# Performance work log

Hardware: AMD Instinct MI355X
Metric: run time of the kernel (lower is better)

Reference implementation:

```python
import jax, jax.numpy as jnp
import numpy as np

N_NODES = 100000
N_EDGES = 1600000
D_IN, D_HID, D_LAT = 128, 128, 64


def setup_inputs() -> dict:
    key = jax.random.key(0)
    ks = jax.random.split(key, 8)
    x = jax.random.normal(ks[0], (N_NODES, D_IN), dtype=jnp.float32)
    edge_index = jax.random.randint(ks[1], (2, N_EDGES), 0, N_NODES, dtype=jnp.int64)
    s1 = 1.0 / np.sqrt(D_IN)
    s2 = 1.0 / np.sqrt(D_HID)
    return {
        "x": x,
        "edge_index": edge_index,
        "W1_l": jax.random.normal(ks[2], (D_IN, D_HID), dtype=jnp.float32) * s1,
        "W1_r": jax.random.normal(ks[3], (D_IN, D_HID), dtype=jnp.float32) * s1,
        "b1": jnp.zeros((D_HID,), dtype=jnp.float32),
        "W2_l": jax.random.normal(ks[4], (D_HID, D_LAT), dtype=jnp.float32) * s2,
        "W2_r": jax.random.normal(ks[5], (D_HID, D_LAT), dtype=jnp.float32) * s2,
        "b2": jnp.zeros((D_LAT,), dtype=jnp.float32),
    }


def _sage_conv_mean(x, src, dst, W_l, W_r, b):
    """PyG SAGEConv with mean aggregation: lin_l(mean_j x_j) + lin_r(x_i)."""
    n = x.shape[0]
    # scatter-mean of source features into destination nodes
    agg = jax.ops.segment_sum(x[src], dst, num_segments=n)           # [N, d]
    deg = jax.ops.segment_sum(jnp.ones_like(dst, dtype=x.dtype), dst, num_segments=n)
    mean = agg / jnp.maximum(deg, 1.0)[:, None]
    return mean @ W_l + b + x @ W_r


def reference(x, edge_index, W1_l, W1_r, b1, W2_l, W2_r, b2):
    src, dst = edge_index[0], edge_index[1]
    h = jax.nn.relu(_sage_conv_mean(x, src, dst, W1_l, W1_r, b1))
    # Dropout(p=0.2) is identity in eval mode
    z = jax.nn.relu(_sage_conv_mean(h, src, dst, W2_l, W2_r, b2))
    return z
```

## Files before the change

### kernel.cpp

```cpp
#include <hip/hip_runtime.h>

#define N_NODES 100000
#define N_EDGES 1600000
#define D_IN 128
#define D_HID 128
#define D_LAT 64

#define BSHIFT 8
#define NB 392
#define CAP 4608
#define EPB 4096
#define PART_BLOCKS ((N_EDGES + EPB - 1) / EPB)
#define CVT_BLOCKS (((long)N_NODES * 128 / 16 + 255) / 256)

typedef unsigned short ushort_t;
typedef unsigned int uint_t;
typedef unsigned char uchar_t;
using bf16x8 = __attribute__((ext_vector_type(8))) short;
using f32x4  = __attribute__((ext_vector_type(4))) float;
using f32x2  = __attribute__((ext_vector_type(2))) float;

__device__ inline ushort_t f2bf(float f) {
    uint_t u = __float_as_uint(f);
    return (ushort_t)((u + 0x7fffu + ((u >> 16) & 1u)) >> 16);
}
__device__ inline uint_t pack2bf(float a, float b) {
    return (uint_t)f2bf(a) | ((uint_t)f2bf(b) << 16);
}
__device__ inline float bf2f(ushort_t u) {
    return __uint_as_float(((uint_t)u) << 16);
}

#if __has_builtin(__builtin_amdgcn_cvt_pk_f32_fp8) && __has_builtin(__builtin_amdgcn_cvt_pk_fp8_f32)
#define HW_FP8 1
template<bool HI>
__device__ inline f32x2 fp8pk2f(uint_t v) {
    return __builtin_amdgcn_cvt_pk_f32_fp8(v, HI);
}
__device__ inline uint_t f2fp8pk4(float a, float b, float c, float d) {
    uint_t w = __builtin_amdgcn_cvt_pk_fp8_f32(a, b, 0, false);
    w = __builtin_amdgcn_cvt_pk_fp8_f32(c, d, w, true);
    return w;
}
__device__ inline uchar_t f2fp8_byte(float f) {
    return (uchar_t)(__builtin_amdgcn_cvt_pk_fp8_f32(f, f, 0, false) & 0xff);
}
#else
__device__ inline float fp8b2f(uint_t b) {
    uint_t em = b & 0x7f;
    if (em == 0) return 0.f;
    uint_t bits = ((em << 20) + (120u << 23)) | ((b & 0x80u) << 24);
    return __uint_as_float(bits);
}
template<bool HI>
__device__ inline f32x2 fp8pk2f(uint_t v) {
    uint_t w = HI ? (v >> 16) : v;
    f32x2 r; r.x = fp8b2f(w & 0xff); r.y = fp8b2f((w >> 8) & 0xff);
    return r;
}
__device__ inline uint_t f2fp8_1(float f) {
    uint_t u = __float_as_uint(f);
    uint_t s = (u >> 31) << 7;
    uint_t au = u & 0x7fffffff;
    if (au >= 0x43e00000u) return s | 0x7e;
    if (au < 0x3c000000u) return s;
    uint_t r = au + 0x0007ffffu + ((au >> 20) & 1u);
    return s | (((r >> 20) - (120u << 3)) & 0x7f);
}
__device__ inline uint_t f2fp8pk4(float a, float b, float c, float d) {
    return f2fp8_1(a) | (f2fp8_1(b) << 8) | (f2fp8_1(c) << 16) | (f2fp8_1(d) << 24);
}
__device__ inline uchar_t f2fp8_byte(float f) { return (uchar_t)f2fp8_1(f); }
#endif

__device__ inline void accf8x4(float* a, uint_t w, int base) {
    f32x2 p0 = fp8pk2f<false>(w);
    f32x2 p1 = fp8pk2f<true>(w);
    a[base + 0] += p0.x; a[base + 1] += p0.y;
    a[base + 2] += p1.x; a[base + 3] += p1.y;
}
__device__ inline void accf8x16(float* a, uint4 u) {
    accf8x4(a, u.x, 0); accf8x4(a, u.y, 4); accf8x4(a, u.z, 8); accf8x4(a, u.w, 12);
}

template<int RSHIFT, int NV, int DEPTH>
__device__ inline void gather_acc_fp8n(const uchar_t* __restrict__ base,
                                       const int* __restrict__ idxp,
                                       int n, float* acc) {
    int k = 0;
    int idx[DEPTH];
    if (n >= DEPTH) {
        #pragma unroll
        for (int j = 0; j < DEPTH; ++j) idx[j] = idxp[j];
    }
    while (k + DEPTH <= n) {
        uint4 u[DEPTH][NV];
        #pragma unroll
        for (int j = 0; j < DEPTH; ++j) {
            #pragma unroll
            for (int v = 0; v < NV; ++v)
                u[j][v] = *(const uint4*)(base + ((long)idx[j] << RSHIFT) + v * 16);
        }
        int kn = k + DEPTH;
        if (kn + DEPTH <= n) {
            #pragma unroll
            for (int j = 0; j < DEPTH; ++j) idx[j] = idxp[kn + j];
        }
        #pragma unroll
        for (int j = 0; j < DEPTH; ++j) {
            #pragma unroll
            for (int v = 0; v < NV; ++v)
                accf8x16(acc + v * 16, u[j][v]);
        }
        k = kn;
    }
    if (k < n) {
        int m = n - k;
        int idr[DEPTH];
        #pragma unroll
        for (int j = 0; j < DEPTH; ++j) {
            int kk = k + j; if (kk > n - 1) kk = n - 1;
            idr[j] = idxp[kk];
        }
        uint4 u[DEPTH][NV];
        #pragma unroll
        for (int j = 0; j < DEPTH; ++j) {
            #pragma unroll
            for (int v = 0; v < NV; ++v)
                u[j][v] = *(const uint4*)(base + ((long)idr[j] << RSHIFT) + v * 16);
        }
        #pragma unroll
        for (int j = 0; j < DEPTH; ++j) {
            if (j < m) {
                #pragma unroll
                for (int v = 0; v < NV; ++v)
                    accf8x16(acc + v * 16, u[j][v]);
            }
        }
    }
}

__device__ inline void pack_w256(const float* Wl, const float* Wr, ushort_t* pack,
                                 int N, int tid) {
    int lane = tid & 63;
    int t = tid >> 6;
    int kt = t & 7;
    int nt = t >> 3;
    int n = nt * 16 + (lane & 15);
    int kbase = kt * 32 + (lane >> 4) * 8;
    ushort_t v[8];
    #pragma unroll
    for (int j = 0; j < 8; ++j) {
        int k = kbase + j;
        float w = (k < 128) ? Wl[k * N + n] : Wr[(k - 128) * N + n];
        v[j] = f2bf(w);
    }
    *(uint4*)(pack + (long)tid * 8) = *(uint4*)v;
}
__device__ inline void pack_w128(const float* W, ushort_t* pack, int N, int tid) {
    int lane = tid & 63;
    int t = tid >> 6;
    int kt = t & 3;
    int nt = t >> 2;
    int n = nt * 16 + (lane & 15);
    int kbase = kt * 32 + (lane >> 4) * 8;
    ushort_t v[8];
    #pragma unroll
    for (int j = 0; j < 8; ++j) v[j] = f2bf(W[(kbase + j) * N + n]);
    *(uint4*)(pack + (long)tid * 8) = *(uint4*)v;
}

__global__ __launch_bounds__(256) void prep_kernel(
        const float* __restrict__ W1_l, const float* __restrict__ W1_r,
        ushort_t* __restrict__ pack1,
        const float* __restrict__ W2_l, ushort_t* __restrict__ pack2l,
        const float* __restrict__ W2_r, ushort_t* __restrict__ pack2r,
        int* __restrict__ gCur,
        const float* __restrict__ x, ushort_t* __restrict__ xb,
        uchar_t* __restrict__ x8) {
    int b = blockIdx.x;
    if (b < 16) {
        pack_w256(W1_l, W1_r, pack1, 128, b * 256 + threadIdx.x);
    } else if (b < 20) {
        pack_w128(W2_l, pack2l, 64, (b - 16) * 256 + threadIdx.x);
    } else if (b < 24) {
        pack_w128(W2_r, pack2r, 64, (b - 20) * 256 + threadIdx.x);
    } else if (b < 26) {
        int t = (b - 24) * 256 + threadIdx.x;
        if (t < NB) gCur[t] = t * CAP;
    } else {
        long i = ((long)(b - 26) * 256 + threadIdx.x) * 16;
        if (i >= (long)N_NODES * 128) return;
        float4 a = *(const float4*)(x + i);
        float4 bb = *(const float4*)(x + i + 4);
        float4 c = *(const float4*)(x + i + 8);
        float4 d = *(const float4*)(x + i + 12);
        uint4 ob0, ob1;
        ob0.x = pack2bf(a.x, a.y);  ob0.y = pack2bf(a.z, a.w);
        ob0.z = pack2bf(bb.x, bb.y); ob0.w = pack2bf(bb.z, bb.w);
        ob1.x = pack2bf(c.x, c.y);  ob1.y = pack2bf(c.z, c.w);
        ob1.z = pack2bf(d.x, d.y);  ob1.w = pack2bf(d.z, d.w);
        *(uint4*)(xb + i) = ob0;
        *(uint4*)(xb + i + 8) = ob1;
        uint4 o8;
        o8.x = f2fp8pk4(a.x, a.y, a.z, a.w);
        o8.y = f2fp8pk4(bb.x, bb.y, bb.z, bb.w);
        o8.z = f2fp8pk4(c.x, c.y, c.z, c.w);
        o8.w = f2fp8pk4(d.x, d.y, d.z, d.w);
        *(uint4*)(x8 + i) = o8;
    }
}

__global__ __launch_bounds__(256) void bucket_scatter_kernel(const int* __restrict__ src,
                                                             const int* __restrict__ dst,
                                                             int* __restrict__ gCur,
                                                             int* __restrict__ bedges) {
    __shared__ int h[NB];
    __shared__ int start[NB];
    for (int j = threadIdx.x; j < NB; j += 256) h[j] = 0;
    __syncthreads();
    long base = (long)blockIdx.x * EPB + threadIdx.x * 16;
    int dc[16], sc[16];
    int cnt = 0;
    if (base + 16 <= N_EDGES) {
        #pragma unroll
        for (int j = 0; j < 4; ++j) {
            int4 d4 = *(const int4*)(dst + base + j * 4);
            int4 s4 = *(const int4*)(src + base + j * 4);
            dc[j * 4 + 0] = d4.x; dc[j * 4 + 1] = d4.y; dc[j * 4 + 2] = d4.z; dc[j * 4 + 3] = d4.w;
            sc[j * 4 + 0] = s4.x; sc[j * 4 + 1] = s4.y; sc[j * 4 + 2] = s4.z; sc[j * 4 + 3] = s4.w;
        }
        cnt = 16;
    } else if (base < N_EDGES) {
        cnt = (int)(N_EDGES - base);
        for (int j = 0; j < cnt; ++j) { dc[j] = dst[base + j]; sc[j] = src[base + j]; }
    }
    for (int j = 0; j < cnt; ++j) atomicAdd(&h[dc[j] >> BSHIFT], 1);
    __syncthreads();
    for (int j = threadIdx.x; j < NB; j += 256)
        start[j] = h[j] ? atomicAdd(&gCur[j], h[j]) : 0;
    __syncthreads();
    for (int j = 0; j < cnt; ++j) {
        int b = dc[j] >> BSHIFT;
        int p = atomicAdd(&start[b], 1);
        if (p < (b + 1) * CAP)
            bedges[p] = ((dc[j] & 255) << 24) | sc[j];
    }
}

__global__ __launch_bounds__(256) void bucket_sort_kernel(const int* __restrict__ gCur,
                                                          const int* __restrict__ bedges,
                                                          int* __restrict__ csr,
                                                          int2* __restrict__ off2) {
    __shared__ int sdata[256];
    __shared__ int cur[256];
    int b = blockIdx.x, t = threadIdx.x;
    int r0 = b * CAP;
    int n = gCur[b] - r0;
    if (n > CAP) n = CAP;
    cur[t] = 0;
    __syncthreads();
    for (int k = t * 4; k < n; k += 1024) {
        int4 v4 = *(const int4*)(bedges + r0 + k);
        int m = n - k;
        atomicAdd(&cur[(unsigned)v4.x >> 24], 1);
        if (m > 1) atomicAdd(&cur[(unsigned)v4.y >> 24], 1);
        if (m > 2) atomicAdd(&cur[(unsigned)v4.z >> 24], 1);
        if (m > 3) atomicAdd(&cur[(unsigned)v4.w >> 24], 1);
    }
    __syncthreads();
    int c = cur[t];
    sdata[t] = c;
    __syncthreads();
    for (int d = 1; d < 256; d <<= 1) {
        int u = (t >= d) ? sdata[t - d] : 0;
        __syncthreads();
        sdata[t] += u;
        __syncthreads();
    }
    int ex = (t == 0) ? 0 : sdata[t - 1];
    off2[(b << BSHIFT) + t] = make_int2(r0 + ex, c);
    cur[t] = ex;
    __syncthreads();
    for (int k = t * 4; k < n; k += 1024) {
        int4 v4 = *(const int4*)(bedges + r0 + k);
        int m = n - k;
        {
            int p = atomicAdd(&cur[(unsigned)v4.x >> 24], 1);
            csr[r0 + p] = v4.x & 0xFFFFFF;
        }
        if (m > 1) {
            int p = atomicAdd(&cur[(unsigned)v4.y >> 24], 1);
            csr[r0 + p] = v4.y & 0xFFFFFF;
        }
        if (m > 2) {
            int p = atomicAdd(&cur[(unsigned)v4.z >> 24], 1);
            csr[r0 + p] = v4.z & 0xFFFFFF;
        }
        if (m > 3) {
            int p = atomicAdd(&cur[(unsigned)v4.w >> 24], 1);
            csr[r0 + p] = v4.w & 0xFFFFFF;
        }
    }
}

#define HSTRIDE 132
__global__ __launch_bounds__(256) void mfma_mlp_fused_kernel(
        const int2* __restrict__ off2, const int* __restrict__ csr_src,
        const uchar_t* __restrict__ x8,
        const ushort_t* __restrict__ Ax,
        const ushort_t* __restrict__ pack1, const float* __restrict__ bias,
        const ushort_t* __restrict__ pack2l,
        ushort_t* __restrict__ hb, uchar_t* __restrict__ g8) {
    __shared__ ushort_t mtile[32 * HSTRIDE];
    __shared__ ushort_t htile[32 * HSTRIDE];
    long m0b = (long)blockIdx.x * 32;
    {
        int lane8 = threadIdx.x & 7;
        int local = threadIdx.x >> 3;
        long i = m0b + local;
        int2 bd = off2[i];
        const uchar_t* gbase = x8 + lane8 * 16;
        float acc[16];
        #pragma unroll
        for (int j = 0; j < 16; ++j) acc[j] = 0.f;
        gather_acc_fp8n<7, 1, 8>(gbase, csr_src + bd.x, bd.y, acc);
        float inv = (bd.y > 0) ? 1.f / (float)bd.y : 0.f;
        uint4 o0, o1;
        o0.x = pack2bf(acc[0] * inv,  acc[1] * inv);
        o0.y = pack2bf(acc[2] * inv,  acc[3] * inv);
        o0.z = pack2bf(acc[4] * inv,  acc[5] * inv);
        o0.w = pack2bf(acc[6] * inv,  acc[7] * inv);
        o1.x = pack2bf(acc[8] * inv,  acc[9] * inv);
        o1.y = pack2bf(acc[10] * inv, acc[11] * inv);
        o1.z = pack2bf(acc[12] * inv, acc[13] * inv);
        o1.w = pack2bf(acc[14] * inv, acc[15] * inv);
        ushort_t* mp = mtile + local * HSTRIDE + lane8 * 16;
        *(uint4*)mp = o0;
        *(uint4*)(mp + 8) = o1;
    }
    __syncthreads();
    int lane = threadIdx.x & 63;
    int wave = threadIdx.x >> 6;
    int wr = wave & 1;
    int wc = wave >> 1;
    int r = lane & 15;
    int quad = lane >> 4;
    int rowl = wr * 16 + r;
    long arow = m0b + rowl;

    bf16x8 areg[8];
    #pragma unroll
    for (int kt = 0; kt < 8; ++kt) {
        int k = (kt & 3) * 32 + quad * 8;
        areg[kt] = (kt < 4)
            ? *(const bf16x8*)(&mtile[rowl * HSTRIDE + k])
            : *(const bf16x8*)(Ax + arow * 128 + k);
    }

    f32x4 acc[4];
    #pragma unroll
    for (int nt = 0; nt < 4; ++nt) acc[nt] = (f32x4){0.f, 0.f, 0.f, 0.f};
    #pragma unroll
    for (int nt = 0; nt < 4; ++nt) {
        int gnt = wc * 4 + nt;
        #pragma unroll
        for (int kt = 0; kt < 8; ++kt) {
            bf16x8 bfrag = *(const bf16x8*)(pack1 + ((long)(gnt * 8 + kt) * 64 + lane) * 8);
            acc[nt] = __builtin_amdgcn_mfma_f32_16x16x32_bf16(areg[kt], bfrag, acc[nt], 0, 0, 0);
        }
    }

    #pragma unroll
    for (int nt = 0; nt < 4; ++nt) {
        int col = wc * 64 + nt * 16 + r;
        float bj = bias[col];
        #pragma unroll
        for (int q = 0; q < 4; ++q) {
            long orow = m0b + wr * 16 + quad * 4 + q;
            float v = fmaxf(acc[nt][q] + bj, 0.f);
            ushort_t hv = f2bf(v);
            hb[orow * 128 + col] = hv;
            htile[(wr * 16 + quad * 4 + q) * HSTRIDE + col] = hv;
        }
    }
    __syncthreads();
    bf16x8 areg2[4];
    #pragma unroll
    for (int kt = 0; kt < 4; ++kt)
        areg2[kt] = *(const bf16x8*)(&htile[rowl * HSTRIDE + kt * 32 + quad * 8]);
    f32x4 gacc[2];
    #pragma unroll
    for (int nt = 0; nt < 2; ++nt) gacc[nt] = (f32x4){0.f, 0.f, 0.f, 0.f};
    #pragma unroll
    for (int nt = 0; nt < 2; ++nt) {
        int gnt = wc * 2 + nt;
        #pragma unroll
        for (int kt = 0; kt < 4; ++kt) {
            bf16x8 bfrag = *(const bf16x8*)(pack2l + ((long)(gnt * 4 + kt) * 64 + lane) * 8);
            gacc[nt] = __builtin_amdgcn_mfma_f32_16x16x32_bf16(areg2[kt], bfrag, gacc[nt], 0, 0, 0);
        }
    }
    #pragma unroll
    for (int nt = 0; nt < 2; ++nt) {
        int col = wc * 32 + nt * 16 + r;
        #pragma unroll
        for (int q = 0; q < 4; ++q) {
            long orow = m0b + wr * 16 + quad * 4 + q;
            g8[orow * 64 + col] = f2fp8_byte(gacc[nt][q]);
        }
    }
}

#define MSTRIDE 68
__global__ __launch_bounds__(256) void mfma_final_kernel(
        const int2* __restrict__ off2, const int* __restrict__ csr_src,
        const uchar_t* __restrict__ g8,
        const ushort_t* __restrict__ hb, const ushort_t* __restrict__ pack2r,
        const float* __restrict__ b2, float* __restrict__ out) {
    __shared__ ushort_t mtile[64 * MSTRIDE];
    long m0 = (long)blockIdx.x * 64;
    {
        int lane  = threadIdx.x & 3;
        int local = threadIdx.x >> 2;
        long i = m0 + local;
        if (i > N_NODES - 1) i = N_NODES - 1;
        int2 bd = off2[i];
        int beg = bd.x, n = bd.y;
        const uchar_t* base = g8 + lane * 16;
        float acc[16];
        #pragma unroll
        for (int j = 0; j < 16; ++j) acc[j] = 0.f;
        gather_acc_fp8n<6, 1, 8>(base, csr_src + beg, n, acc);
        float inv = (n > 0) ? 1.f / (float)n : 0.f;
        uint4 o0, o1;
        o0.x = pack2bf(acc[0] * inv,  acc[1] * inv);
        o0.y = pack2bf(acc[2] * inv,  acc[3] * inv);
        o0.z = pack2bf(acc[4] * inv,  acc[5] * inv);
        o0.w = pack2bf(acc[6] * inv,  acc[7] * inv);
        o1.x = pack2bf(acc[8] * inv,  acc[9] * inv);
        o1.y = pack2bf(acc[10] * inv, acc[11] * inv);
        o1.z = pack2bf(acc[12] * inv, acc[13] * inv);
        o1.w = pack2bf(acc[14] * inv, acc[15] * inv);
        ushort_t* mp = mtile + local * MSTRIDE + lane * 16;
        *(uint4*)mp = o0;
        *(uint4*)(mp + 8) = o1;
    }
    __syncthreads();
    int lane = threadIdx.x & 63;
    int wave = threadIdx.x >> 6;
    long mw = m0 + wave * 16;
    int r = lane & 15;
    int quad = lane >> 4;
    long arow = mw + r;
    if (arow > N_NODES - 1) arow = N_NODES - 1;

    bf16x8 areg[4];
    #pragma unroll
    for (int kt = 0; kt < 4; ++kt)
        areg[kt] = *(const bf16x8*)(hb + arow * 128 + kt * 32 + quad * 8);

    f32x4 acc[4];
    #pragma unroll
    for (int nt = 0; nt < 4; ++nt) {
        int col = nt * 16 + r;
        #pragma unroll
        for (int q = 0; q < 4; ++q) {
            int rowl = wave * 16 + quad * 4 + q;
            acc[nt][q] = bf2f(mtile[rowl * MSTRIDE + col]);
        }
    }
    #pragma unroll
    for (int nt = 0; nt < 4; ++nt) {
        #pragma unroll
        for (int kt = 0; kt < 4; ++kt) {
            bf16x8 bfrag = *(const bf16x8*)(pack2r + ((long)(nt * 4 + kt) * 64 + lane) * 8);
            acc[nt] = __builtin_amdgcn_mfma_f32_16x16x32_bf16(areg[kt], bfrag, acc[nt], 0, 0, 0);
        }
    }
    #pragma unroll
    for (int nt = 0; nt < 4; ++nt) {
        int col = nt * 16 + r;
        float bj = b2[col];
        #pragma unroll
        for (int q = 0; q < 4; ++q) {
            long orow = mw + quad * 4 + q;
            if (orow < N_NODES)
                out[orow * 64 + col] = fmaxf(acc[nt][q] + bj, 0.f);
        }
    }
}

extern "C" void kernel_launch(void* const* d_in, const int* in_sizes, int n_in,
                              void* d_out, int out_size, void* d_ws, size_t ws_size,
                              hipStream_t stream) {
    const float* x    = (const float*)d_in[0];
    const int*   ei   = (const int*)d_in[1];
    const float* W1_l = (const float*)d_in[2];
    const float* W1_r = (const float*)d_in[3];
    const float* b1   = (const float*)d_in[4];
    const float* W2_l = (const float*)d_in[5];
    const float* W2_r = (const float*)d_in[6];
    const float* b2   = (const float*)d_in[7];
    float* out = (float*)d_out;

    const int* src = ei;
    const int* dst = ei + N_EDGES;

    int*  gCur   = (int*)d_ws;
    int2* off2   = (int2*)(gCur + 512);
    int*  bedges = (int*)(off2 + 100608);
    int*  csr    = bedges + NB * CAP;
    ushort_t* xb = (ushort_t*)(csr + NB * CAP);
    ushort_t* hb = xb + (long)N_NODES * 128;
    uchar_t*  x8 = (uchar_t*)(hb + (long)N_NODES * 128);
    ushort_t* pack1  = (ushort_t*)(x8 + (long)N_NODES * 128);
    ushort_t* pack2l = pack1 + 256 * 128;
    ushort_t* pack2r = pack2l + 128 * 64;
    uchar_t*  g8     = (uchar_t*)(pack2r + 128 * 64);

    prep_kernel<<<26 + CVT_BLOCKS, 256, 0, stream>>>(
        W1_l, W1_r, pack1, W2_l, pack2l, W2_r, pack2r, gCur, x, xb, x8);

    bucket_scatter_kernel<<<PART_BLOCKS, 256, 0, stream>>>(src, dst, gCur, bedges);
    bucket_sort_kernel<<<NB, 256, 0, stream>>>(gCur, bedges, csr, off2);

    mfma_mlp_fused_kernel<<<N_NODES / 32, 256, 0, stream>>>(
        off2, csr, x8, xb, pack1, b1, pack2l, hb, g8);

    mfma_final_kernel<<<(N_NODES + 63) / 64, 256, 0, stream>>>(
        off2, csr, g8, hb, pack2r, b2, out);
}
```

Baseline: 232.5 us.

## Fuse layer-2 root projection into layer-1 kernel and split final gather across lanes

The layer-2 root term h@W2_r is now computed in the fused MLP kernel while h is still in shared memory and stored as a 64-wide bf16 tensor. The 128-wide bf16 h buffer is no longer written or re-read. The final kernel becomes a pure gather-mean plus add, bias and relu, with no MFMA. It splits each node's neighbor list across two lane groups with a strided index walk and combines them by shuffle, so more lanes are busy per node. The cost is extra MFMA work and registers in the fused kernel, and a strided index access pattern in the gather.

Measured after the change: 229.1 us. No clear change (-1.5%).

```diff
diff --git a/kernel.cpp b/kernel.cpp
--- a/kernel.cpp
+++ b/kernel.cpp
@@ -83,7 +83,7 @@
     accf8x4(a, u.x, 0); accf8x4(a, u.y, 4); accf8x4(a, u.z, 8); accf8x4(a, u.w, 12);
 }
 
-template<int RSHIFT, int NV, int DEPTH>
+template<int RSHIFT, int NV, int DEPTH, int STRIDE = 1>
 __device__ inline void gather_acc_fp8n(const uchar_t* __restrict__ base,
                                        const int* __restrict__ idxp,
                                        int n, float* acc) {
@@ -91,7 +91,7 @@
     int idx[DEPTH];
     if (n >= DEPTH) {
         #pragma unroll
-        for (int j = 0; j < DEPTH; ++j) idx[j] = idxp[j];
+        for (int j = 0; j < DEPTH; ++j) idx[j] = idxp[j * STRIDE];
     }
     while (k + DEPTH <= n) {
         uint4 u[DEPTH][NV];
@@ -104,7 +104,7 @@
         int kn = k + DEPTH;
         if (kn + DEPTH <= n) {
             #pragma unroll
-            for (int j = 0; j < DEPTH; ++j) idx[j] = idxp[kn + j];
+            for (int j = 0; j < DEPTH; ++j) idx[j] = idxp[(kn + j) * STRIDE];
         }
         #pragma unroll
         for (int j = 0; j < DEPTH; ++j) {
@@ -120,7 +120,7 @@
         #pragma unroll
         for (int j = 0; j < DEPTH; ++j) {
             int kk = k + j; if (kk > n - 1) kk = n - 1;
-            idr[j] = idxp[kk];
+            idr[j] = idxp[kk * STRIDE];
         }
         uint4 u[DEPTH][NV];
         #pragma unroll
@@ -310,8 +310,8 @@
         const uchar_t* __restrict__ x8,
         const ushort_t* __restrict__ Ax,
         const ushort_t* __restrict__ pack1, const float* __restrict__ bias,
-        const ushort_t* __restrict__ pack2l,
-        ushort_t* __restrict__ hb, uchar_t* __restrict__ g8) {
+        const ushort_t* __restrict__ pack2l, const ushort_t* __restrict__ pack2r,
+        ushort_t* __restrict__ f2, uchar_t* __restrict__ g8) {
     __shared__ ushort_t mtile[32 * HSTRIDE];
     __shared__ ushort_t htile[32 * HSTRIDE];
     long m0b = (long)blockIdx.x * 32;
@@ -377,11 +377,8 @@
         float bj = bias[col];
         #pragma unroll
         for (int q = 0; q < 4; ++q) {
-            long orow = m0b + wr * 16 + quad * 4 + q;
             float v = fmaxf(acc[nt][q] + bj, 0.f);
-            ushort_t hv = f2bf(v);
-            hb[orow * 128 + col] = hv;
-            htile[(wr * 16 + quad * 4 + q) * HSTRIDE + col] = hv;
+            htile[(wr * 16 + quad * 4 + q) * HSTRIDE + col] = f2bf(v);
         }
     }
     __syncthreads();
@@ -410,85 +407,61 @@
             g8[orow * 64 + col] = f2fp8_byte(gacc[nt][q]);
         }
     }
-}
-
-#define MSTRIDE 68
-__global__ __launch_bounds__(256) void mfma_final_kernel(
+    f32x4 facc[2];
+    #pragma unroll
+    for (int nt = 0; nt < 2; ++nt) facc[nt] = (f32x4){0.f, 0.f, 0.f, 0.f};
+    #pragma unroll
+    for (int nt = 0; nt < 2; ++nt) {
+        int gnt = wc * 2 + nt;
+        #pragma unroll
+        for (int kt = 0; kt < 4; ++kt) {
+            bf16x8 bfrag = *(const bf16x8*)(pack2r + ((long)(gnt * 4 + kt) * 64 + lane) * 8);
+            facc[nt] = __builtin_amdgcn_mfma_f32_16x16x32_bf16(areg2[kt], bfrag, facc[nt], 0, 0, 0);
+        }
+    }
+    #pragma unroll
+    for (int nt = 0; nt < 2; ++nt) {
+        int col = wc * 32 + nt * 16 + r;
+        #pragma unroll
+        for (int q = 0; q < 4; ++q) {
+            long orow = m0b + wr * 16 + quad * 4 + q;
+            f2[orow * 64 + col] = f2bf(facc[nt][q]);
+        }
+    }
+}
+
+__global__ __launch_bounds__(256) void final_gather_kernel(
         const int2* __restrict__ off2, const int* __restrict__ csr_src,
         const uchar_t* __restrict__ g8,
-        const ushort_t* __restrict__ hb, const ushort_t* __restrict__ pack2r,
-        const float* __restrict__ b2, float* __restrict__ out) {
-    __shared__ ushort_t mtile[64 * MSTRIDE];
-    long m0 = (long)blockIdx.x * 64;
-    {
-        int lane  = threadIdx.x & 3;
-        int local = threadIdx.x >> 2;
-        long i = m0 + local;
-        if (i > N_NODES - 1) i = N_NODES - 1;
-        int2 bd = off2[i];
-        int beg = bd.x, n = bd.y;
-        const uchar_t* base = g8 + lane * 16;
-        float acc[16];
-        #pragma unroll
-        for (int j = 0; j < 16; ++j) acc[j] = 0.f;
-        gather_acc_fp8n<6, 1, 8>(base, csr_src + beg, n, acc);
-        float inv = (n > 0) ? 1.f / (float)n : 0.f;
-        uint4 o0, o1;
-        o0.x = pack2bf(acc[0] * inv,  acc[1] * inv);
-        o0.y = pack2bf(acc[2] * inv,  acc[3] * inv);
-        o0.z = pack2bf(acc[4] * inv,  acc[5] * inv);
-        o0.w = pack2bf(acc[6] * inv,  acc[7] * inv);
-        o1.x = pack2bf(acc[8] * inv,  acc[9] * inv);
-        o1.y = pack2bf(acc[10] * inv, acc[11] * inv);
-        o1.z = pack2bf(acc[12] * inv, acc[13] * inv);
-        o1.w = pack2bf(acc[14] * inv, acc[15] * inv);
-        ushort_t* mp = mtile + local * MSTRIDE + lane * 16;
-        *(uint4*)mp = o0;
-        *(uint4*)(mp + 8) = o1;
-    }
-    __syncthreads();
-    int lane = threadIdx.x & 63;
-    int wave = threadIdx.x >> 6;
-    long mw = m0 + wave * 16;
-    int r = lane & 15;
-    int quad = lane >> 4;
-    long arow = mw + r;
-    if (arow > N_NODES - 1) arow = N_NODES - 1;
-
-    bf16x8 areg[4];
-    #pragma unroll
-    for (int kt = 0; kt < 4; ++kt)
-        areg[kt] = *(const bf16x8*)(hb + arow * 128 + kt * 32 + quad * 8);
-
-    f32x4 acc[4];
-    #pragma unroll
-    for (int nt = 0; nt < 4; ++nt) {
-        int col = nt * 16 + r;
-        #pragma unroll
-        for (int q = 0; q < 4; ++q) {
-            int rowl = wave * 16 + quad * 4 + q;
-            acc[nt][q] = bf2f(mtile[rowl * MSTRIDE + col]);
-        }
-    }
-    #pragma unroll
-    for (int nt = 0; nt < 4; ++nt) {
-        #pragma unroll
-        for (int kt = 0; kt < 4; ++kt) {
-            bf16x8 bfrag = *(const bf16x8*)(pack2r + ((long)(nt * 4 + kt) * 64 + lane) * 8);
-            acc[nt] = __builtin_amdgcn_mfma_f32_16x16x32_bf16(areg[kt], bfrag, acc[nt], 0, 0, 0);
-        }
-    }
-    #pragma unroll
-    for (int nt = 0; nt < 4; ++nt) {
-        int col = nt * 16 + r;
-        float bj = b2[col];
-        #pragma unroll
-        for (int q = 0; q < 4; ++q) {
-            long orow = mw + quad * 4 + q;
-            if (orow < N_NODES)
-                out[orow * 64 + col] = fmaxf(acc[nt][q] + bj, 0.f);
-        }
-    }
+        const ushort_t* __restrict__ f2, const float* __restrict__ b2,
+        float* __restrict__ out) {
+    int lane8 = threadIdx.x & 7;
+    int d = lane8 & 3;
+    int p = lane8 >> 2;
+    int local = threadIdx.x >> 3;
+    long i = (long)blockIdx.x * 32 + local;
+    int2 bd = off2[i];
+    int n = bd.y;
+    const uchar_t* base = g8 + d * 16;
+    float acc[16];
+    #pragma unroll
+    for (int j = 0; j < 16; ++j) acc[j] = 0.f;
+    int np = (n + 1 - p) >> 1;
+    gather_acc_fp8n<6, 1, 8, 2>(base, csr_src + bd.x + p, np, acc);
+    #pragma unroll
+    for (int j = 0; j < 16; ++j) acc[j] += __shfl_xor(acc[j], 4);
+    float inv = (n > 0) ? 1.f / (float)n : 0.f;
+    int dim0 = d * 16 + p * 8;
+    ushort_t fu[8];
+    *(uint4*)fu = *(const uint4*)(f2 + i * 64 + dim0);
+    float o[8];
+    #pragma unroll
+    for (int j = 0; j < 8; ++j) {
+        float m = bf2f(f2bf(acc[p * 8 + j] * inv));
+        o[j] = fmaxf(m + bf2f(fu[j]) + b2[dim0 + j], 0.f);
+    }
+    *(float4*)(out + i * 64 + dim0)     = make_float4(o[0], o[1], o[2], o[3]);
+    *(float4*)(out + i * 64 + dim0 + 4) = make_float4(o[4], o[5], o[6], o[7]);
 }
 
 extern "C" void kernel_launch(void* const* d_in, const int* in_sizes, int n_in,
@@ -512,9 +485,9 @@
     int*  bedges = (int*)(off2 + 100608);
     int*  csr    = bedges + NB * CAP;
     ushort_t* xb = (ushort_t*)(csr + NB * CAP);
-    ushort_t* hb = xb + (long)N_NODES * 128;
-    uchar_t*  x8 = (uchar_t*)(hb + (long)N_NODES * 128);
-    ushort_t* pack1  = (ushort_t*)(x8 + (long)N_NODES * 128);
+    uchar_t*  x8 = (uchar_t*)(xb + (long)N_NODES * 128);
+    ushort_t* f2 = (ushort_t*)(x8 + (long)N_NODES * 128);
+    ushort_t* pack1  = f2 + (long)N_NODES * 64;
     ushort_t* pack2l = pack1 + 256 * 128;
     ushort_t* pack2r = pack2l + 128 * 64;
     uchar_t*  g8     = (uchar_t*)(pack2r + 128 * 64);
@@ -526,8 +499,8 @@
     bucket_sort_kernel<<<NB, 256, 0, stream>>>(gCur, bedges, csr, off2);
 
     mfma_mlp_fused_kernel<<<N_NODES / 32, 256, 0, stream>>>(
-        off2, csr, x8, xb, pack1, b1, pack2l, hb, g8);
-
-    mfma_final_kernel<<<(N_NODES + 63) / 64, 256, 0, stream>>>(
-        off2, csr, g8, hb, pack2r, b2, out);
-}
+        off2, csr, x8, xb, pack1, b1, pack2l, pack2r, f2, g8);
+
+    final_gather_kernel<<<N_NODES / 32, 256, 0, stream>>>(
+        off2, csr, g8, f2, b2, out);
+}
```
